# Performance work log

Measured on AMD Instinct MI355X. Metric: run time of the kernel, lower is better.

Reference implementation:

```python
import jax, jax.numpy as jnp
import numpy as np

K = 16  # neighbors

def setup_inputs() -> dict:
    key = jax.random.key(0)
    x = jax.random.normal(key, (2, 8192, 64), dtype=jnp.float32)
    return {"x": x}

def reference(x):
    # pairwise squared euclidean distance: ||xi||^2 - 2 xi.xj + ||xj||^2
    b, n, d = x.shape
    x_inner = -2.0 * jnp.einsum('bnd,bmd->bnm', x, x)          # (B,N,N)
    x_sq = jnp.sum(x * x, axis=-1, keepdims=True)               # (B,N,1)
    dist = x_sq + x_inner + jnp.swapaxes(x_sq, 1, 2)            # (B,N,N)
    # torch.topk(-dist, k) -> largest of -dist == k nearest neighbors
    _, nn_idx = jax.lax.top_k(-dist, K)                         # (B,N,K) int32
    center_idx = jnp.broadcast_to(jnp.arange(n, dtype=nn_idx.dtype)[None, :, None], (b, n, K))
    return jnp.stack((nn_idx, center_idx), axis=0)              # (2,B,N,K)
```

## Files before the change

### kernel.cpp

```cpp
#include <hip/hip_runtime.h>
#include <stdint.h>

constexpr int N_   = 8192;
constexpr int D_   = 64;
constexpr int K_   = 16;
constexpr int NQ   = 16384;
constexpr int MS   = 8;
constexpr int CAPB = 32;
constexpr float SLOP = 0.012f;

typedef __attribute__((ext_vector_type(8))) short bf16x8;
typedef __attribute__((ext_vector_type(4))) float f32x4;

template<int JN>
__device__ __forceinline__ void topk_insertf(float (&key)[JN], float nk) {
    if (nk < key[JN - 1]) {
        bool c[JN];
#pragma unroll
        for (int j = 0; j < JN; ++j) c[j] = nk < key[j];
#pragma unroll
        for (int j = JN - 1; j >= 1; --j)
            key[j] = c[j - 1] ? key[j - 1] : (c[j] ? nk : key[j]);
        key[0] = c[0] ? nk : key[0];
    }
}

__device__ __forceinline__ unsigned short bf16_rne(float f) {
    uint32_t u = __float_as_uint(f);
    return (unsigned short)((u + 0x7FFFu + ((u >> 16) & 1u)) >> 16);
}

__device__ __forceinline__ void gl_lds16(const void* g, void* l) {
    __builtin_amdgcn_global_load_lds(
        (const __attribute__((address_space(1))) unsigned int*)g,
        (__attribute__((address_space(3))) unsigned int*)l, 16, 0, 0);
}

#define SWZ(r, s) (((r) << 7) + ((((s) ^ ((r) & 7))) << 4))

__global__ void __launch_bounds__(256) split_k(const float* __restrict__ x,
                                               unsigned short* __restrict__ xh,
                                               unsigned short* __restrict__ xl,
                                               float* __restrict__ nrm) {
    const int t = blockIdx.x * 256 + (int)threadIdx.x;
    const int row = t >> 4, seg = t & 15;
    const float4 v = reinterpret_cast<const float4*>(x)[t];
    float f[4] = {v.x, v.y, v.z, v.w};
    unsigned short h[4], l[4];
    float sq = 0.f;
#pragma unroll
    for (int j = 0; j < 4; ++j) {
        sq = fmaf(f[j], f[j], sq);
        h[j] = bf16_rne(f[j]);
        float hf = __uint_as_float((uint32_t)h[j] << 16);
        l[j] = bf16_rne(f[j] - hf);
    }
    sq += __shfl_xor(sq, 1, 16); sq += __shfl_xor(sq, 2, 16);
    sq += __shfl_xor(sq, 4, 16); sq += __shfl_xor(sq, 8, 16);
    if (seg == 0) nrm[row] = sq;
    ushort4 hv = {h[0], h[1], h[2], h[3]}, lv = {l[0], l[1], l[2], l[3]};
    reinterpret_cast<ushort4*>(xh)[t] = hv;
    reinterpret_cast<ushort4*>(xl)[t] = lv;
}

__global__ void __launch_bounds__(256) tau_p(const unsigned short* __restrict__ xh,
                                             const unsigned short* __restrict__ xl,
                                             const float* __restrict__ nrm,
                                             float* __restrict__ part) {
    __shared__ alignas(16) unsigned short A[64 * 64];
    __shared__ alignas(16) unsigned short Bb[256 * 64];
    __shared__ float nrmb[128];
    const int tid = (int)threadIdx.x;
    const int q0g = (int)blockIdx.x * 32;
    const int b   = q0g >> 13;
    const int n0  = q0g & (N_ - 1);
    const unsigned short* __restrict__ xhb = xh + (size_t)b * N_ * D_;
    const unsigned short* __restrict__ xlb = xl + (size_t)b * N_ * D_;
    const float* __restrict__ nb = nrm + b * N_;

#pragma unroll
    for (int k = 0; k < 2; ++k) {
        int u = tid + k * 256, r = u >> 3, s = u & 7;
        const unsigned short* src = (r < 32) ? xhb + (size_t)(n0 + r) * D_
                                             : xlb + (size_t)(n0 + r - 32) * D_;
        *(float4*)((char*)A + SWZ(r, s)) = *(const float4*)((const char*)src + (s << 4));
    }

    const int wave = tid >> 6, lane = tid & 63;
    const int l15 = lane & 15, quad = lane >> 4;

    float lad0[8], lad1[8];
#pragma unroll
    for (int j = 0; j < 8; ++j) { lad0[j] = __builtin_inff(); lad1[j] = __builtin_inff(); }

    for (int mc = 0; mc < 16; ++mc) {
        const int m0 = mc * 128;
        __syncthreads();
#pragma unroll
        for (int k = 0; k < 8; ++k) {
            int u = tid + k * 256, r = u >> 3, s = u & 7;
            const unsigned short* src = (r < 128) ? xhb + (size_t)(m0 + r) * D_
                                                  : xlb + (size_t)(m0 + r - 128) * D_;
            *(float4*)((char*)Bb + SWZ(r, s)) = *(const float4*)((const char*)src + (s << 4));
        }
        if (tid < 128) nrmb[tid] = nb[m0 + tid];
        __syncthreads();

        f32x4 acc[2][2] = {};
#pragma unroll
        for (int half = 0; half < 2; ++half) {
            const int seg = half * 4 + quad;
            bf16x8 afh[2], afl[2], bfh[2], bfl[2];
#pragma unroll
            for (int tm = 0; tm < 2; ++tm) {
                afh[tm] = *(const bf16x8*)((const char*)A + SWZ(tm * 16 + l15, seg));
                afl[tm] = *(const bf16x8*)((const char*)A + SWZ(32 + tm * 16 + l15, seg));
            }
#pragma unroll
            for (int tn = 0; tn < 2; ++tn) {
                bfh[tn] = *(const bf16x8*)((const char*)Bb + SWZ(wave * 32 + tn * 16 + l15, seg));
                bfl[tn] = *(const bf16x8*)((const char*)Bb + SWZ(128 + wave * 32 + tn * 16 + l15, seg));
            }
#pragma unroll
            for (int tm = 0; tm < 2; ++tm)
#pragma unroll
                for (int tn = 0; tn < 2; ++tn) {
                    acc[tm][tn] = __builtin_amdgcn_mfma_f32_16x16x32_bf16(afh[tm], bfh[tn], acc[tm][tn], 0, 0, 0);
                    acc[tm][tn] = __builtin_amdgcn_mfma_f32_16x16x32_bf16(afh[tm], bfl[tn], acc[tm][tn], 0, 0, 0);
                    acc[tm][tn] = __builtin_amdgcn_mfma_f32_16x16x32_bf16(afl[tm], bfh[tn], acc[tm][tn], 0, 0, 0);
                }
        }
#pragma unroll
        for (int tn = 0; tn < 2; ++tn) {
            const float nm = nrmb[wave * 32 + tn * 16 + l15];
#pragma unroll
            for (int tm = 0; tm < 2; ++tm)
#pragma unroll
                for (int reg = 0; reg < 4; ++reg) {
                    float keyf = fmaf(-2.f, acc[tm][tn][reg], nm);
                    const int li = tm * 4 + reg;
                    float k0 = lad0[li];
                    lad0[li] = fminf(k0, keyf);
                    lad1[li] = fminf(fmaxf(keyf, k0), lad1[li]);
                }
        }
    }
#pragma unroll
    for (int tm = 0; tm < 2; ++tm)
#pragma unroll
        for (int reg = 0; reg < 4; ++reg) {
            const int r = tm * 16 + quad * 4 + reg;
            const int li = tm * 4 + reg;
            float2 v = {lad0[li], lad1[li]};
            *(float2*)(part + ((size_t)(q0g + r)) * 128 + (wave * 16 + l15) * 2) = v;
        }
}

__global__ void __launch_bounds__(64) tau_m(const float* __restrict__ part,
                                            float* __restrict__ tau) {
    const int q = blockIdx.x * 64 + (int)threadIdx.x;
    const float4* p = reinterpret_cast<const float4*>(part + (size_t)q * 128);
    float key[K_];
#pragma unroll
    for (int j = 0; j < K_; ++j) key[j] = __builtin_inff();
    for (int i = 0; i < 32; ++i) {
        float4 v = p[i];
        topk_insertf<K_>(key, v.x); topk_insertf<K_>(key, v.y);
        topk_insertf<K_>(key, v.z); topk_insertf<K_>(key, v.w);
    }
    tau[q] = key[15] + SLOP;
}

__global__ void __launch_bounds__(256, 2) filter_k(const unsigned short* __restrict__ xh,
                                                   const unsigned short* __restrict__ xl,
                                                   const float* __restrict__ nrm,
                                                   const float* __restrict__ tau,
                                                   unsigned short* __restrict__ cnt_pb,
                                                   unsigned short* __restrict__ buf2) {
    __shared__ alignas(16) unsigned short A[256 * 64];
    __shared__ alignas(16) unsigned short Bb[256 * 64];
    __shared__ alignas(16) float taub[128];
    __shared__ alignas(16) float nrmS[1024];
    __shared__ unsigned short lists[128 * CAPB];
    __shared__ unsigned int cntL[128];
    const int tid = (int)threadIdx.x;
    const int bid = (int)blockIdx.x;
    const int b  = bid >> 9;
    const int qt = (bid >> 3) & 63;
    const int ms = bid & 7;
    const int q0 = qt * 128;
    const unsigned short* __restrict__ xhb = xh + (size_t)b * N_ * D_;
    const unsigned short* __restrict__ xlb = xl + (size_t)b * N_ * D_;
    const float* __restrict__ nb = nrm + b * N_;
    const int w = tid >> 6;

#pragma unroll
    for (int k = 0; k < 8; ++k) {
        int u = k * 256 + tid, r = u >> 3, sg = (u & 7) ^ (r & 7);
        const unsigned short* src = (r < 128) ? xhb + (size_t)(q0 + r) * D_
                                              : xlb + (size_t)(q0 + r - 128) * D_;
        gl_lds16((const char*)src + (sg << 4), (char*)A + (k << 12) + (w << 10));
    }
    {
        const int m0 = ms * 1024;
#pragma unroll
        for (int k = 0; k < 8; ++k) {
            int u = k * 256 + tid, r = u >> 3, sg = (u & 7) ^ (r & 7);
            const unsigned short* src = (r < 128) ? xhb + (size_t)(m0 + r) * D_
                                                  : xlb + (size_t)(m0 + r - 128) * D_;
            gl_lds16((const char*)src + (sg << 4), (char*)Bb + (k << 12) + (w << 10));
        }
    }
    *(float4*)(nrmS + tid * 4) = *(const float4*)(nb + ms * 1024 + tid * 4);
    if (tid < 128) { cntL[tid] = 0; taub[tid] = tau[(b << 13) + q0 + tid]; }
    __syncthreads();

    const int lane = tid & 63;
    const int wq = w >> 1, wm = w & 1;
    const int l15 = lane & 15, quad = lane >> 4;

    for (int mc = 0; mc < 8; ++mc) {
        f32x4 acc[4][4] = {};
#pragma unroll
        for (int half = 0; half < 2; ++half) {
            const int seg = half * 4 + quad;
            bf16x8 afh[4], afl[4], bfh[4], bfl[4];
#pragma unroll
            for (int tm = 0; tm < 4; ++tm) {
                afh[tm] = *(const bf16x8*)((const char*)A + SWZ(wq * 64 + tm * 16 + l15, seg));
                afl[tm] = *(const bf16x8*)((const char*)A + SWZ(128 + wq * 64 + tm * 16 + l15, seg));
            }
#pragma unroll
            for (int tn = 0; tn < 4; ++tn) {
                bfh[tn] = *(const bf16x8*)((const char*)Bb + SWZ(wm * 64 + tn * 16 + l15, seg));
                bfl[tn] = *(const bf16x8*)((const char*)Bb + SWZ(128 + wm * 64 + tn * 16 + l15, seg));
            }
#pragma unroll
            for (int tm = 0; tm < 4; ++tm)
#pragma unroll
                for (int tn = 0; tn < 4; ++tn) {
                    acc[tm][tn] = __builtin_amdgcn_mfma_f32_16x16x32_bf16(afh[tm], bfh[tn], acc[tm][tn], 0, 0, 0);
                    acc[tm][tn] = __builtin_amdgcn_mfma_f32_16x16x32_bf16(afh[tm], bfl[tn], acc[tm][tn], 0, 0, 0);
                    acc[tm][tn] = __builtin_amdgcn_mfma_f32_16x16x32_bf16(afl[tm], bfh[tn], acc[tm][tn], 0, 0, 0);
                }
        }

        float nmv[4]; int mlv[4];
#pragma unroll
        for (int tn = 0; tn < 4; ++tn) {
            mlv[tn] = mc * 128 + wm * 64 + tn * 16 + l15;
            nmv[tn] = nrmS[mlv[tn]];
        }
        f32x4 t4v[4];
#pragma unroll
        for (int tm = 0; tm < 4; ++tm) {
            f32x4 t4 = *(const f32x4*)(taub + wq * 64 + tm * 16 + quad * 4);
            t4v[tm] = t4 + SLOP;
        }
#pragma unroll
        for (int tm = 0; tm < 4; ++tm)
#pragma unroll
            for (int tn = 0; tn < 4; ++tn)
#pragma unroll
                for (int reg = 0; reg < 4; ++reg) {
                    float keyf = fmaf(-2.f, acc[tm][tn][reg], nmv[tn]);
                    if (keyf <= t4v[tm][reg]) {
                        int ql = wq * 64 + tm * 16 + quad * 4 + reg;
                        unsigned pos = atomicAdd(&cntL[ql], 1u);
                        if (pos < CAPB) lists[ql * CAPB + pos] = (unsigned short)(ms * 1024 + mlv[tn]);
                    }
                }

        __syncthreads();
        if (mc < 7) {
            const int m0n = ms * 1024 + (mc + 1) * 128;
#pragma unroll
            for (int k = 0; k < 8; ++k) {
                int u = k * 256 + tid, r = u >> 3, sg = (u & 7) ^ (r & 7);
                const unsigned short* src = (r < 128) ? xhb + (size_t)(m0n + r) * D_
                                                      : xlb + (size_t)(m0n + r - 128) * D_;
                gl_lds16((const char*)src + (sg << 4), (char*)Bb + (k << 12) + (w << 10));
            }
        }
        __syncthreads();
    }
    if (tid < 128) {
        int q = (b << 13) + q0 + tid;
        unsigned cn = cntL[tid]; cn = cn < CAPB ? cn : CAPB;
        cnt_pb[(size_t)q * MS + ms] = (unsigned short)cn;
        unsigned short* dst = buf2 + ((size_t)q * MS + ms) * CAPB;
        for (unsigned i = 0; i < cn; ++i) dst[i] = lists[tid * CAPB + i];
    }
}

__global__ void __launch_bounds__(256) rerank_k(const float* __restrict__ x,
                                                const unsigned short* __restrict__ cnt_pb,
                                                const unsigned short* __restrict__ buf2,
                                                int* __restrict__ out) {
    __shared__ float Qs[4 * 64];
    __shared__ unsigned short ids[4 * MS * CAPB];
    const int tid = (int)threadIdx.x;
    const int w = tid >> 6, lane = tid & 63;
    const int q = blockIdx.x * 4 + w;
    const int b = q >> 13, n = q & (N_ - 1);
    const float* __restrict__ xb = x + (size_t)b * N_ * D_;
    Qs[w * 64 + lane] = xb[(size_t)n * D_ + lane];

    int off[MS + 1]; off[0] = 0;
#pragma unroll
    for (int ms = 0; ms < MS; ++ms) {
        int c = (int)cnt_pb[(size_t)q * MS + ms]; c = c < CAPB ? c : CAPB;
        off[ms + 1] = off[ms] + c;
    }
    const int total = off[MS];
    for (int idx = lane; idx < total; idx += 64) {
        int ms = 0;
#pragma unroll
        for (int t = 1; t < MS; ++t) ms += (idx >= off[t]) ? 1 : 0;
        ids[(w * MS) * CAPB + idx] = buf2[((size_t)q * MS + ms) * CAPB + (idx - off[ms])];
    }
    __syncthreads();

    unsigned long long v = ~0ull;
    int consumed = 0;
    bool first = true;
    while (first || consumed < total) {
        const int myIdx = first ? lane : consumed + lane - 16;
        const bool take = (first || lane >= 16) && myIdx < total;
        unsigned long long nk = ~0ull;
        if (take) {
            const int id = (int)ids[(w * MS) * CAPB + myIdx];
            const float* __restrict__ crow = xb + (size_t)id * D_;
            double a0 = 0.0, a1 = 0.0, a2 = 0.0, a3 = 0.0;
#pragma unroll
            for (int j = 0; j < 16; ++j) {
                const float4 c  = *(const float4*)(crow + j * 4);
                const float4 qv = *(const float4*)(Qs + w * 64 + j * 4);
                double d0 = (double)qv.x - (double)c.x; a0 = fma(d0, d0, a0);
                double d1 = (double)qv.y - (double)c.y; a1 = fma(d1, d1, a1);
                double d2 = (double)qv.z - (double)c.z; a2 = fma(d2, d2, a2);
                double d3 = (double)qv.w - (double)c.w; a3 = fma(d3, d3, a3);
            }
            double s = (a0 + a1) + (a2 + a3);
            nk = ((unsigned long long)__double_as_longlong(s) & ~0x1FFFull) | (unsigned)id;
        }
        if (first || lane >= 16) v = nk;
#pragma unroll
        for (int k = 2; k <= 64; k <<= 1)
#pragma unroll
            for (int j = k >> 1; j > 0; j >>= 1) {
                unsigned long long o = __shfl_xor(v, j, 64);
                const bool keepmin = (((lane & k) == 0) == ((lane & j) == 0));
                unsigned long long mn = v < o ? v : o;
                unsigned long long mx = v < o ? o : v;
                v = keepmin ? mn : mx;
            }
        consumed += first ? 64 : 48;
        first = false;
    }
    if (lane < K_) {
        out[(size_t)q * K_ + lane]                   = (int)(v & 0x1FFFull);
        out[(size_t)NQ * K_ + (size_t)q * K_ + lane] = n;
    }
}

extern "C" void kernel_launch(void* const* d_in, const int* in_sizes, int n_in,
                              void* d_out, int out_size, void* d_ws, size_t ws_size,
                              hipStream_t stream) {
    const float* x = (const float*)d_in[0];
    int* out = (int*)d_out;
    char* ws = (char*)d_ws;
    float*          nrm    = (float*)ws;
    float*          tau    = (float*)(ws + (64 << 10));
    unsigned short* cnt_pb = (unsigned short*)(ws + (128 << 10));
    unsigned short* xh     = (unsigned short*)(ws + (1 << 20));
    unsigned short* xl     = (unsigned short*)(ws + (3 << 20));
    unsigned short* buf2   = (unsigned short*)(ws + (5 << 20));
    float*          part   = (float*)(ws + (5 << 20));

    hipLaunchKernelGGL(split_k,  dim3(1024), dim3(256), 0, stream, x, xh, xl, nrm);
    hipLaunchKernelGGL(tau_p,    dim3(512),  dim3(256), 0, stream, xh, xl, nrm, part);
    hipLaunchKernelGGL(tau_m,    dim3(256),  dim3(64),  0, stream, part, tau);
    hipLaunchKernelGGL(filter_k, dim3(1024), dim3(256), 0, stream, xh, xl, nrm, tau, cnt_pb, buf2);
    hipLaunchKernelGGL(rerank_k, dim3(4096), dim3(256), 0, stream, x, cnt_pb, buf2, out);
}
```

Baseline: 242.2 us.

## Double-buffer B tiles in filter kernel and hoist A fragments into registers

Splits the candidate tile into 64-row chunks held in two LDS buffers, so the next chunk's global-to-LDS copy is issued before the current chunk's MFMA work. This overlaps memory transfer with compute and drops one barrier per iteration. The A fragments and the per-query thresholds are now loaded into registers once instead of every iteration. The cost is more registers for the hoisted fragments, which may lower occupancy, and twice as many smaller iterations each with less MFMA work.

Result: no change. 242.5 us (+0.1%).

```diff
diff --git a/kernel.cpp b/kernel.cpp
--- a/kernel.cpp
+++ b/kernel.cpp
@@ -178,7 +178,7 @@
                                                    unsigned short* __restrict__ cnt_pb,
                                                    unsigned short* __restrict__ buf2) {
     __shared__ alignas(16) unsigned short A[256 * 64];
-    __shared__ alignas(16) unsigned short Bb[256 * 64];
+    __shared__ alignas(16) unsigned short Bd[2][128 * 64];
     __shared__ alignas(16) float taub[128];
     __shared__ alignas(16) float nrmS[1024];
     __shared__ unsigned short lists[128 * CAPB];
@@ -204,11 +204,11 @@
     {
         const int m0 = ms * 1024;
 #pragma unroll
-        for (int k = 0; k < 8; ++k) {
+        for (int k = 0; k < 4; ++k) {
             int u = k * 256 + tid, r = u >> 3, sg = (u & 7) ^ (r & 7);
-            const unsigned short* src = (r < 128) ? xhb + (size_t)(m0 + r) * D_
-                                                  : xlb + (size_t)(m0 + r - 128) * D_;
-            gl_lds16((const char*)src + (sg << 4), (char*)Bb + (k << 12) + (w << 10));
+            const unsigned short* src = (r < 64) ? xhb + (size_t)(m0 + r) * D_
+                                                 : xlb + (size_t)(m0 + r - 64) * D_;
+            gl_lds16((const char*)src + (sg << 4), (char*)Bd[0] + (k << 12) + (w << 10));
         }
     }
     *(float4*)(nrmS + tid * 4) = *(const float4*)(nb + ms * 1024 + tid * 4);
@@ -219,48 +219,64 @@
     const int wq = w >> 1, wm = w & 1;
     const int l15 = lane & 15, quad = lane >> 4;
 
-    for (int mc = 0; mc < 8; ++mc) {
-        f32x4 acc[4][4] = {};
+    bf16x8 Afh[2][4], Afl[2][4];
+#pragma unroll
+    for (int half = 0; half < 2; ++half) {
+        const int seg = half * 4 + quad;
+#pragma unroll
+        for (int tm = 0; tm < 4; ++tm) {
+            Afh[half][tm] = *(const bf16x8*)((const char*)A + SWZ(wq * 64 + tm * 16 + l15, seg));
+            Afl[half][tm] = *(const bf16x8*)((const char*)A + SWZ(128 + wq * 64 + tm * 16 + l15, seg));
+        }
+    }
+    f32x4 t4v[4];
+#pragma unroll
+    for (int tm = 0; tm < 4; ++tm)
+        t4v[tm] = *(const f32x4*)(taub + wq * 64 + tm * 16 + quad * 4) + SLOP;
+
+    for (int mc = 0; mc < 16; ++mc) {
+        const int cur = mc & 1;
+        if (mc < 15) {
+            const int m0n = ms * 1024 + (mc + 1) * 64;
+#pragma unroll
+            for (int k = 0; k < 4; ++k) {
+                int u = k * 256 + tid, r = u >> 3, sg = (u & 7) ^ (r & 7);
+                const unsigned short* src = (r < 64) ? xhb + (size_t)(m0n + r) * D_
+                                                     : xlb + (size_t)(m0n + r - 64) * D_;
+                gl_lds16((const char*)src + (sg << 4), (char*)Bd[1 - cur] + (k << 12) + (w << 10));
+            }
+        }
+
+        f32x4 acc[4][2] = {};
 #pragma unroll
         for (int half = 0; half < 2; ++half) {
             const int seg = half * 4 + quad;
-            bf16x8 afh[4], afl[4], bfh[4], bfl[4];
-#pragma unroll
-            for (int tm = 0; tm < 4; ++tm) {
-                afh[tm] = *(const bf16x8*)((const char*)A + SWZ(wq * 64 + tm * 16 + l15, seg));
-                afl[tm] = *(const bf16x8*)((const char*)A + SWZ(128 + wq * 64 + tm * 16 + l15, seg));
-            }
-#pragma unroll
-            for (int tn = 0; tn < 4; ++tn) {
-                bfh[tn] = *(const bf16x8*)((const char*)Bb + SWZ(wm * 64 + tn * 16 + l15, seg));
-                bfl[tn] = *(const bf16x8*)((const char*)Bb + SWZ(128 + wm * 64 + tn * 16 + l15, seg));
+            bf16x8 bfh[2], bfl[2];
+#pragma unroll
+            for (int tn = 0; tn < 2; ++tn) {
+                bfh[tn] = *(const bf16x8*)((const char*)Bd[cur] + SWZ(wm * 32 + tn * 16 + l15, seg));
+                bfl[tn] = *(const bf16x8*)((const char*)Bd[cur] + SWZ(64 + wm * 32 + tn * 16 + l15, seg));
             }
 #pragma unroll
             for (int tm = 0; tm < 4; ++tm)
 #pragma unroll
-                for (int tn = 0; tn < 4; ++tn) {
-                    acc[tm][tn] = __builtin_amdgcn_mfma_f32_16x16x32_bf16(afh[tm], bfh[tn], acc[tm][tn], 0, 0, 0);
-                    acc[tm][tn] = __builtin_amdgcn_mfma_f32_16x16x32_bf16(afh[tm], bfl[tn], acc[tm][tn], 0, 0, 0);
-                    acc[tm][tn] = __builtin_amdgcn_mfma_f32_16x16x32_bf16(afl[tm], bfh[tn], acc[tm][tn], 0, 0, 0);
+                for (int tn = 0; tn < 2; ++tn) {
+                    acc[tm][tn] = __builtin_amdgcn_mfma_f32_16x16x32_bf16(Afh[half][tm], bfh[tn], acc[tm][tn], 0, 0, 0);
+                    acc[tm][tn] = __builtin_amdgcn_mfma_f32_16x16x32_bf16(Afh[half][tm], bfl[tn], acc[tm][tn], 0, 0, 0);
+                    acc[tm][tn] = __builtin_amdgcn_mfma_f32_16x16x32_bf16(Afl[half][tm], bfh[tn], acc[tm][tn], 0, 0, 0);
                 }
         }
 
-        float nmv[4]; int mlv[4];
-#pragma unroll
-        for (int tn = 0; tn < 4; ++tn) {
-            mlv[tn] = mc * 128 + wm * 64 + tn * 16 + l15;
+        float nmv[2]; int mlv[2];
+#pragma unroll
+        for (int tn = 0; tn < 2; ++tn) {
+            mlv[tn] = mc * 64 + wm * 32 + tn * 16 + l15;
             nmv[tn] = nrmS[mlv[tn]];
         }
-        f32x4 t4v[4];
-#pragma unroll
-        for (int tm = 0; tm < 4; ++tm) {
-            f32x4 t4 = *(const f32x4*)(taub + wq * 64 + tm * 16 + quad * 4);
-            t4v[tm] = t4 + SLOP;
-        }
 #pragma unroll
         for (int tm = 0; tm < 4; ++tm)
 #pragma unroll
-            for (int tn = 0; tn < 4; ++tn)
+            for (int tn = 0; tn < 2; ++tn)
 #pragma unroll
                 for (int reg = 0; reg < 4; ++reg) {
                     float keyf = fmaf(-2.f, acc[tm][tn][reg], nmv[tn]);
@@ -271,17 +287,6 @@
                     }
                 }
 
-        __syncthreads();
-        if (mc < 7) {
-            const int m0n = ms * 1024 + (mc + 1) * 128;
-#pragma unroll
-            for (int k = 0; k < 8; ++k) {
-                int u = k * 256 + tid, r = u >> 3, sg = (u & 7) ^ (r & 7);
-                const unsigned short* src = (r < 128) ? xhb + (size_t)(m0n + r) * D_
-                                                      : xlb + (size_t)(m0n + r - 128) * D_;
-                gl_lds16((const char*)src + (sg << 4), (char*)Bb + (k << 12) + (w << 10));
-            }
-        }
         __syncthreads();
     }
     if (tid < 128) {
```
